# Kernel optimization log

Measured on AMD Instinct MI355X. Metric: run time of the kernel, lower is better.

## Reference

```python
import jax, jax.numpy as jnp
import numpy as np

H = 16  # n_heads from init_kwargs


def setup_inputs() -> dict:
    key = jax.random.key(0)
    ks = jax.random.split(key, 9)
    B, N, D = 4, 4096, 1024
    mk = lambda k, shape: jax.random.normal(k, shape, dtype=jnp.float32) * 0.02
    return {
        "x": jax.random.normal(ks[0], (B, N, D), dtype=jnp.float32),
        "Wq": mk(ks[1], (D, D)), "bq": mk(ks[2], (D,)),
        "Wk": mk(ks[3], (D, D)), "bk": mk(ks[4], (D,)),
        "Wv": mk(ks[5], (D, D)), "bv": mk(ks[6], (D,)),
        "Wo": mk(ks[7], (D, D)), "bo": mk(ks[8], (D,)),
    }


def _split_heads(t):
    B, N, D = t.shape
    return t.reshape(B, N, H, D // H).transpose(0, 2, 1, 3)  # b h n d


def reference(x, Wq, bq, Wk, bk, Wv, bv, Wo, bo):
    B, N, D = x.shape
    d_head = D // H
    s = (d_head ** 0.5) ** (-0.25)
    q = _split_heads(x @ Wq + bq)
    # NOTE: original computes key(x) but immediately overwrites it with
    # q.softmax(dim=-2); key projection is dead code. We replicate exactly.
    _ = x @ Wk + bk  # dead, kept for parameter-shape parity
    v = _split_heads(x @ Wv + bv)
    q = jax.nn.softmax(q, axis=-1) * s            # softmax over d_head
    k = jax.nn.softmax(q, axis=-2) * s            # softmax of q over seq dim (faithful!)
    ctx = jnp.einsum('bhnd,bhne->bhde', k, v)     # k^T @ v, [B,H,d,d]
    attn = jnp.einsum('bhnd,bhde->bhne', q, ctx)  # q @ ctx, [B,H,N,d]
    attn = attn.transpose(0, 2, 1, 3).reshape(B, N, D)
    # n_heads > 1 -> to_out linear; dropout is identity in eval mode
    return attn @ Wo + bo
```

## Files before the change

kernel.cpp:

```cpp
#include <hip/hip_runtime.h>

typedef unsigned short u16;
typedef __attribute__((ext_vector_type(8))) short short8;
typedef __attribute__((ext_vector_type(4))) float f4;
typedef __attribute__((ext_vector_type(8))) unsigned short us8;

__device__ __forceinline__ u16 f2bf(float f) {
    unsigned u = __float_as_uint(f);
    u += 0x7FFFu + ((u >> 16) & 1u);
    return (u16)(u >> 16);
}
__device__ __forceinline__ float bf2f(u16 h) {
    return __uint_as_float(((unsigned)h) << 16);
}

#define GLD16(gp, lp) __builtin_amdgcn_global_load_lds( \
    (const __attribute__((address_space(1))) void*)(gp), \
    (__attribute__((address_space(3))) void*)(lp), 16, 0, 0)

#define SCALE_S 0.594603557501360533f

__global__ __launch_bounds__(256) void convert_f32_bf16(const float* __restrict__ in,
                                                        u16* __restrict__ out) {
    const size_t i = (size_t)blockIdx.x * 256 + threadIdx.x;
    const float4* p = (const float4*)in + i * 2;
    float4 a = p[0], b = p[1];
    us8 r;
    r[0] = f2bf(a.x); r[1] = f2bf(a.y); r[2] = f2bf(a.z); r[3] = f2bf(a.w);
    r[4] = f2bf(b.x); r[5] = f2bf(b.y); r[6] = f2bf(b.z); r[7] = f2bf(b.w);
    *(us8*)(out + i * 8) = r;
}

__global__ __launch_bounds__(256) void transpose_convert3(
    const float* __restrict__ Wq, const float* __restrict__ Wv, const float* __restrict__ Wo,
    u16* __restrict__ WqvT, u16* __restrict__ WoT) {
    const float* W; u16* out;
    if (blockIdx.z == 0)      { W = Wq; out = WqvT; }
    else if (blockIdx.z == 1) { W = Wv; out = WqvT + 1024 * 1024; }
    else                      { W = Wo; out = WoT; }
    __shared__ float tile[32][33];
    const int tx = threadIdx.x, ty = threadIdx.y;
    const int x = blockIdx.x * 32 + tx;
#pragma unroll
    for (int i = 0; i < 4; ++i) {
        const int y = blockIdx.y * 32 + ty + i * 8;
        tile[ty + i * 8][tx] = W[(size_t)y * 1024 + x];
    }
    __syncthreads();
#pragma unroll
    for (int i = 0; i < 4; ++i) {
        const int yo = blockIdx.x * 32 + ty + i * 8;
        const int xo = blockIdx.y * 32 + tx;
        out[(size_t)yo * 1024 + xo] = f2bf(tile[tx][ty + i * 8]);
    }
}

__global__ void concat_bias(const float* __restrict__ bq, const float* __restrict__ bv,
                            float* __restrict__ bqv) {
    const int i = blockIdx.x * 256 + threadIdx.x;
    bqv[i] = (i < 1024) ? bq[i] : bv[i - 1024];
}

#define BAR8() do { asm volatile("" ::: "memory"); __builtin_amdgcn_s_barrier(); \
                    asm volatile("" ::: "memory"); } while (0)
#define WAITV(n) asm volatile("s_waitcnt vmcnt(" #n ")" ::: "memory")

#define STG2(arr, p, half) do { \
    const u16* s_ = (p) + (size_t)(half) * 128 * 1024; \
    u16* d_ = &arr[half][ldst]; \
    GLD16(s_, d_); \
    GLD16(s_ + (size_t)64 * 1024, d_ + 64 * 64); \
} while (0)

#define MFMA_CL(base) \
    _Pragma("unroll") for (int kk_ = 0; kk_ < 2; ++kk_) \
    _Pragma("unroll") for (int i_ = 0; i_ < 4; ++i_) \
    _Pragma("unroll") for (int j_ = 0; j_ < 4; ++j_) \
        acc[(base) + i_][j_] = __builtin_amdgcn_mfma_f32_16x16x32_bf16( \
            bf[j_][kk_], af[i_][kk_], acc[(base) + i_][j_], 0, 0, 0);

#define KTILE(AsR, BsR, AsW, BsW) do { \
    short8 bf[4][2]; \
    _Pragma("unroll") for (int j_ = 0; j_ < 4; ++j_) \
    _Pragma("unroll") for (int kk_ = 0; kk_ < 2; ++kk_) \
        bf[j_][kk_] = *(const short8*)&BsR[bhalf][(brow + j_ * 16 + lrow) * 64 + (kg0 ^ (kk_ << 5))]; \
    { \
        short8 af[4][2]; \
        _Pragma("unroll") for (int i_ = 0; i_ < 4; ++i_) \
        _Pragma("unroll") for (int kk_ = 0; kk_ < 2; ++kk_) \
            af[i_][kk_] = *(const short8*)&AsR[wrow][(i_ * 16 + lrow) * 64 + (kg0 ^ (kk_ << 5))]; \
        STG2(AsW, aP, 0); STG2(AsW, aP, 1); aP += 64; \
        __builtin_amdgcn_s_setprio(1); \
        MFMA_CL(0) \
        __builtin_amdgcn_s_setprio(0); \
    } \
    { \
        short8 af[4][2]; \
        _Pragma("unroll") for (int i_ = 0; i_ < 4; ++i_) \
        _Pragma("unroll") for (int kk_ = 0; kk_ < 2; ++kk_) \
            af[i_][kk_] = *(const short8*)&AsR[wrow][((64 + i_ * 16 + lrow)) * 64 + (kg0 ^ (kk_ << 5))]; \
        BAR8(); \
        STG2(BsW, bP, 0); STG2(BsW, bP, 1); bP += 64; \
        __builtin_amdgcn_s_setprio(1); \
        MFMA_CL(4) \
        __builtin_amdgcn_s_setprio(0); \
    } \
    WAITV(4); \
    BAR8(); \
} while (0)

#define KTILE_NOSYNC(AsR, BsR) do { \
    short8 bf[4][2]; \
    _Pragma("unroll") for (int j_ = 0; j_ < 4; ++j_) \
    _Pragma("unroll") for (int kk_ = 0; kk_ < 2; ++kk_) \
        bf[j_][kk_] = *(const short8*)&BsR[bhalf][(brow + j_ * 16 + lrow) * 64 + (kg0 ^ (kk_ << 5))]; \
    _Pragma("unroll") for (int h_ = 0; h_ < 2; ++h_) { \
        short8 af[4][2]; \
        _Pragma("unroll") for (int i_ = 0; i_ < 4; ++i_) \
        _Pragma("unroll") for (int kk_ = 0; kk_ < 2; ++kk_) \
            af[i_][kk_] = *(const short8*)&AsR[wrow][((h_ * 64 + i_ * 16 + lrow)) * 64 + (kg0 ^ (kk_ << 5))]; \
        if (h_ == 0) { MFMA_CL(0) } else { MFMA_CL(4) } \
    } \
} while (0)

__global__ __launch_bounds__(512, 2) void gemm_qv(
    const u16* __restrict__ A, const u16* __restrict__ BT,
    const float* __restrict__ bias,
    u16* __restrict__ qsOut, u16* __restrict__ vOut)
{
    __shared__ u16 As0[2][128 * 64], As1[2][128 * 64];
    __shared__ u16 Bs0[2][128 * 64], Bs1[2][128 * 64];
    const int t = threadIdx.x;
    const int l = t & 63, w = t >> 6;
    const int quad = l >> 4, lrow = l & 15;
    const int wrow = w >> 2, wcol = w & 3;
    const int bhalf = wcol >> 1, brow = (wcol & 1) * 64;

    int bx, by;
    {
        const int id = blockIdx.x + (int)gridDim.x * blockIdx.y;
        const int xcd = id & 7, j = id >> 3;
        const int xs = (int)gridDim.x >> 3;
        bx = xcd * xs + (j % xs);
        by = j / xs;
    }
    const int m0 = bx * 256, n0 = by * 256;

    const int lr0 = t >> 3;
    const int cg = ((t & 7) ^ (lr0 & 7)) * 8;
    const int ldst = lr0 * 64 + (t & 7) * 8;
    const u16* aS = A  + (size_t)(m0 + lr0) * 1024 + cg;
    const u16* bS = BT + (size_t)(n0 + lr0) * 1024 + cg;

    const int kg0 = (quad ^ (lrow & 7)) << 3;
    f4 acc[8][4] = {};

    STG2(Bs0, bS, 0); STG2(Bs0, bS, 1);
    STG2(As0, aS, 0); STG2(As0, aS, 1);
    {
        const u16* b1 = bS + 64;
        STG2(Bs1, b1, 0); STG2(Bs1, b1, 1);
    }
    WAITV(4);
    BAR8();

    const u16* aP = aS + 64;
    const u16* bP = bS + 128;

    for (int kt2 = 0; kt2 < 7; ++kt2) {
        KTILE(As0, Bs0, As1, Bs0);
        KTILE(As1, Bs1, As0, Bs1);
    }
    STG2(As1, aP, 0); STG2(As1, aP, 1);
    WAITV(0);
    BAR8();
    KTILE_NOSYNC(As0, Bs0);
    KTILE_NOSYNC(As1, Bs1);

    const int colh = n0 + wcol * 64;
    const bool isQ = n0 < 1024;
    float4 bs4[4];
#pragma unroll
    for (int j = 0; j < 4; ++j)
        bs4[j] = *(const float4*)&bias[colh + j * 16 + quad * 4];

#pragma unroll
    for (int i = 0; i < 8; ++i) {
        const int m = m0 + wrow * 128 + i * 16 + lrow;
        float v[4][4];
#pragma unroll
        for (int j = 0; j < 4; ++j) {
            v[j][0] = acc[i][j][0] + bs4[j].x;
            v[j][1] = acc[i][j][1] + bs4[j].y;
            v[j][2] = acc[i][j][2] + bs4[j].z;
            v[j][3] = acc[i][j][3] + bs4[j].w;
        }
        if (isQ) {
            float mx = v[0][0];
#pragma unroll
            for (int j = 0; j < 4; ++j)
#pragma unroll
                for (int r = 0; r < 4; ++r) mx = fmaxf(mx, v[j][r]);
            mx = fmaxf(mx, __shfl_xor(mx, 16));
            mx = fmaxf(mx, __shfl_xor(mx, 32));
            float sm = 0.f;
#pragma unroll
            for (int j = 0; j < 4; ++j)
#pragma unroll
                for (int r = 0; r < 4; ++r) { v[j][r] = __expf(v[j][r] - mx); sm += v[j][r]; }
            sm += __shfl_xor(sm, 16);
            sm += __shfl_xor(sm, 32);
            const float inv = SCALE_S / sm;
            u16* qp = qsOut + (size_t)m * 1024 + colh + quad * 4;
#pragma unroll
            for (int j = 0; j < 4; ++j) {
                uint2 pk;
                pk.x = (unsigned)f2bf(v[j][0] * inv) | ((unsigned)f2bf(v[j][1] * inv) << 16);
                pk.y = (unsigned)f2bf(v[j][2] * inv) | ((unsigned)f2bf(v[j][3] * inv) << 16);
                *(uint2*)(qp + j * 16) = pk;
            }
        } else {
            u16* vp = vOut + (size_t)m * 1024 + (colh - 1024) + quad * 4;
#pragma unroll
            for (int j = 0; j < 4; ++j) {
                uint2 pk;
                pk.x = (unsigned)f2bf(v[j][0]) | ((unsigned)f2bf(v[j][1]) << 16);
                pk.y = (unsigned)f2bf(v[j][2]) | ((unsigned)f2bf(v[j][3]) << 16);
                *(uint2*)(vp + j * 16) = pk;
            }
        }
    }
}

__global__ __launch_bounds__(512, 2) void gemm_out(
    const u16* __restrict__ A, const u16* __restrict__ BT,
    const float* __restrict__ bias, float* __restrict__ C)
{
    __shared__ u16 As0[2][128 * 64], As1[2][128 * 64];
    __shared__ u16 Bs0[2][128 * 64], Bs1[2][128 * 64];
    const int t = threadIdx.x;
    const int l = t & 63, w = t >> 6;
    const int quad = l >> 4, lrow = l & 15;
    const int wrow = w >> 2, wcol = w & 3;
    const int bhalf = wcol >> 1, brow = (wcol & 1) * 64;
    const int z = blockIdx.z;
    A  += (size_t)z * (4096 * 1024);
    BT += (size_t)z * (1024 * 1024);
    C  += (size_t)z * (4096 * 1024);

    int bx, by;
    {
        const int id = blockIdx.x + (int)gridDim.x * blockIdx.y;
        const int xcd = id & 7, j = id >> 3;
        const int xs = (int)gridDim.x >> 3;
        bx = xcd * xs + (j % xs);
        by = j / xs;
    }
    const int m0 = bx * 256, n0 = by * 256;

    const int lr0 = t >> 3;
    const int cg = ((t & 7) ^ (lr0 & 7)) * 8;
    const int ldst = lr0 * 64 + (t & 7) * 8;
    const u16* aS = A  + (size_t)(m0 + lr0) * 1024 + cg;
    const u16* bS = BT + (size_t)(n0 + lr0) * 1024 + cg;

    const int kg0 = (quad ^ (lrow & 7)) << 3;
    f4 acc[8][4] = {};

    STG2(Bs0, bS, 0); STG2(Bs0, bS, 1);
    STG2(As0, aS, 0); STG2(As0, aS, 1);
    {
        const u16* b1 = bS + 64;
        STG2(Bs1, b1, 0); STG2(Bs1, b1, 1);
    }
    WAITV(4);
    BAR8();

    const u16* aP = aS + 64;
    const u16* bP = bS + 128;

    for (int kt2 = 0; kt2 < 7; ++kt2) {
        KTILE(As0, Bs0, As1, Bs0);
        KTILE(As1, Bs1, As0, Bs1);
    }
    STG2(As1, aP, 0); STG2(As1, aP, 1);
    WAITV(0);
    BAR8();
    KTILE_NOSYNC(As0, Bs0);
    KTILE_NOSYNC(As1, Bs1);

    const int colh = n0 + wcol * 64;
    float4 bs4[4];
#pragma unroll
    for (int j = 0; j < 4; ++j)
        bs4[j] = *(const float4*)&bias[colh + j * 16 + quad * 4];
#pragma unroll
    for (int i = 0; i < 8; ++i) {
        const int m = m0 + wrow * 128 + i * 16 + lrow;
        float* cp = C + (size_t)m * 1024 + colh + quad * 4;
#pragma unroll
        for (int j = 0; j < 4; ++j) {
            float4 o;
            o.x = acc[i][j][0] + bs4[j].x;
            o.y = acc[i][j][1] + bs4[j].y;
            o.z = acc[i][j][2] + bs4[j].z;
            o.w = acc[i][j][3] + bs4[j].w;
            *(float4*)(cp + j * 16) = o;
        }
    }
}

__global__ __launch_bounds__(256) void ctx_mfma(
    const u16* __restrict__ qs, const u16* __restrict__ vb,
    float* __restrict__ Mpart, float* __restrict__ Zpart)
{
    __shared__ __align__(16) u16 Et[2][64 * 64];
    __shared__ __align__(16) u16 Vt[2][64 * 64];
    const int t = threadIdx.x;
    const int w = t >> 6, l = t & 63;
    const int quad = l >> 4, lrow = l & 15;
    const int g = blockIdx.x;
    const int split = blockIdx.y;
    const int b = g >> 4, h = g & 15;

    const int n0 = (l & 31) * 2;
    const int d0 = w * 16 + (l >> 5) * 8;
    const u16* qp = qs + ((size_t)b * 4096 + (size_t)split * 256 + n0) * 1024 + h * 64 + d0;
    const u16* vp = vb + ((size_t)b * 4096 + (size_t)split * 256 + n0) * 1024 + h * 64 + d0;

    f4 acc[4] = {};
    float zacc[8] = {};

    us8 q8a = *(const us8*)qp;
    us8 q8b = *(const us8*)(qp + 1024);
    us8 v8a = *(const us8*)vp;
    us8 v8b = *(const us8*)(vp + 1024);

    for (int slab = 0; slab < 4; ++slab) {
        unsigned epk[8], vpk[8];
#pragma unroll
        for (int j = 0; j < 8; ++j) {
            float ea = __expf(bf2f((u16)q8a[j]));
            float eb = __expf(bf2f((u16)q8b[j]));
            zacc[j] += ea + eb;
            epk[j] = (unsigned)f2bf(ea) | ((unsigned)f2bf(eb) << 16);
            vpk[j] = (unsigned)(u16)v8a[j] | ((unsigned)(u16)v8b[j] << 16);
        }
        if (slab < 3) {
            qp += 64 * 1024; vp += 64 * 1024;
            q8a = *(const us8*)qp;  q8b = *(const us8*)(qp + 1024);
            v8a = *(const us8*)vp;  v8b = *(const us8*)(vp + 1024);
        }
        u16* et = Et[slab & 1];
        u16* vt = Vt[slab & 1];
#pragma unroll
        for (int j = 0; j < 8; ++j) {
            const int d = d0 + j;
            const int off = d * 64 + (((n0 >> 3) ^ (d & 7)) << 3) + (n0 & 7);
            *(unsigned*)&et[off] = epk[j];
            *(unsigned*)&vt[off] = vpk[j];
        }
        __syncthreads();
#pragma unroll
        for (int kk = 0; kk < 2; ++kk) {
            const int blk = ((kk * 4 + quad) ^ (lrow & 7)) << 3;
            short8 a = *(const short8*)&et[(w * 16 + lrow) * 64 + blk];
#pragma unroll
            for (int j = 0; j < 4; ++j) {
                short8 bfr = *(const short8*)&vt[(j * 16 + lrow) * 64 + blk];
                acc[j] = __builtin_amdgcn_mfma_f32_16x16x32_bf16(bfr, a, acc[j], 0, 0, 0);
            }
        }
    }

#pragma unroll
    for (int j = 0; j < 8; ++j) {
        zacc[j] += __shfl_xor(zacc[j], 1);
        zacc[j] += __shfl_xor(zacc[j], 2);
        zacc[j] += __shfl_xor(zacc[j], 4);
        zacc[j] += __shfl_xor(zacc[j], 8);
        zacc[j] += __shfl_xor(zacc[j], 16);
    }
    if ((l & 31) == 0) {
        float* zp = Zpart + ((size_t)split * 64 + g) * 64 + d0;
#pragma unroll
        for (int j = 0; j < 8; ++j) zp[j] = zacc[j];
    }

    float* mp = Mpart + ((size_t)split * 64 + g) * 4096;
#pragma unroll
    for (int j = 0; j < 4; ++j) {
        float4 o;
        o.x = acc[j][0]; o.y = acc[j][1]; o.z = acc[j][2]; o.w = acc[j][3];
        *(float4*)&mp[(w * 16 + lrow) * 64 + j * 16 + quad * 4] = o;
    }
}

__global__ __launch_bounds__(256) void ctx_norm(const float* __restrict__ Mpart,
                                                const float* __restrict__ Zpart,
                                                float* __restrict__ ctx2) {
    const int g = blockIdx.x, t = threadIdx.x;
    __shared__ float rz[64];
    if (t < 64) {
        float zsum = 0.f;
#pragma unroll
        for (int s = 0; s < 16; ++s) zsum += Zpart[((size_t)s * 64 + g) * 64 + t];
        rz[t] = SCALE_S / zsum;
    }
    __syncthreads();
    for (int idx = t; idx < 4096; idx += 256) {
        float m = 0.f;
#pragma unroll
        for (int s = 0; s < 16; ++s) m += Mpart[((size_t)s * 64 + g) * 4096 + idx];
        ctx2[(size_t)g * 4096 + idx] = m * rz[idx >> 6];
    }
}

__global__ __launch_bounds__(256) void woprime(const float* __restrict__ ctx2,
                                               const u16* __restrict__ WoT,
                                               u16* __restrict__ WopT) {
    __shared__ float ctxT[64 * 65];
    __shared__ __align__(16) u16 wo[64 * 64];
    const int t = threadIdx.x;
    const int jt = blockIdx.x, h = blockIdx.y, b = blockIdx.z;
    const int g = b * 16 + h;
    for (int idx = t; idx < 4096; idx += 256) {
        const int d = idx >> 6, e = idx & 63;
        ctxT[e * 65 + d] = ctx2[(size_t)g * 4096 + idx];
    }
    const int j0 = jt * 64;
#pragma unroll
    for (int c = 0; c < 2; ++c) {
        const int ii = c * 256 + t;
        const int j = ii >> 3, c8 = ii & 7;
        *(us8*)&wo[j * 64 + c8 * 8] = *(const us8*)&WoT[(size_t)(j0 + j) * 1024 + h * 64 + c8 * 8];
    }
    __syncthreads();
    const int d = t & 63, w = t >> 6;
    float accj[16] = {};
    for (int eb = 0; eb < 8; ++eb) {
        float c8[8];
#pragma unroll
        for (int e = 0; e < 8; ++e) c8[e] = ctxT[(eb * 8 + e) * 65 + d];
#pragma unroll
        for (int jj = 0; jj < 16; ++jj) {
            us8 w8 = *(const us8*)&wo[(jj * 4 + w) * 64 + eb * 8];
#pragma unroll
            for (int e = 0; e < 8; ++e)
                accj[jj] += bf2f((u16)w8[e]) * c8[e];
        }
    }
#pragma unroll
    for (int jj = 0; jj < 16; ++jj)
        WopT[(size_t)b * 1048576 + (size_t)(j0 + jj * 4 + w) * 1024 + h * 64 + d] = f2bf(accj[jj]);
}

extern "C" void kernel_launch(void* const* d_in, const int* in_sizes, int n_in,
                              void* d_out, int out_size, void* d_ws, size_t ws_size,
                              hipStream_t stream)
{
    const float* x  = (const float*)d_in[0];
    const float* Wq = (const float*)d_in[1];
    const float* bq = (const float*)d_in[2];
    const float* Wv = (const float*)d_in[5];
    const float* bv = (const float*)d_in[6];
    const float* Wo = (const float*)d_in[7];
    const float* bo = (const float*)d_in[8];
    float* out = (float*)d_out;

    char* ws = (char*)d_ws;
    size_t o = 0;
    auto alloc = [&](size_t bytes) { char* p = ws + o; o = (o + bytes + 255) & ~(size_t)255; return p; };
    u16*   x_bf  = (u16*)  alloc(16384ull * 1024 * 2);
    u16*   WqvT  = (u16*)  alloc(2048ull * 1024 * 2);
    u16*   WoT   = (u16*)  alloc(1024ull * 1024 * 2);
    float* bqv   = (float*)alloc(2048ull * 4);
    u16*   qs    = (u16*)  alloc(16384ull * 1024 * 2);
    u16*   vbuf  = (u16*)  alloc(16384ull * 1024 * 2);
    float* Zpart = (float*)alloc(16ull * 64 * 64 * 4);
    float* ctx2  = (float*)alloc(64ull * 4096 * 4);
    u16*   WopT  = (u16*)  alloc(4ull * 1024 * 1024 * 2);
    float* Mpart = (float*)x_bf;
    (void)ws_size; (void)in_sizes; (void)n_in; (void)out_size;

    convert_f32_bf16<<<8192, 256, 0, stream>>>(x, x_bf);
    transpose_convert3<<<dim3(32, 32, 3), dim3(32, 8), 0, stream>>>(Wq, Wv, Wo, WqvT, WoT);
    concat_bias<<<8, 256, 0, stream>>>(bq, bv, bqv);

    gemm_qv<<<dim3(64, 8), 512, 0, stream>>>(x_bf, WqvT, bqv, qs, vbuf);
    ctx_mfma<<<dim3(64, 16), 256, 0, stream>>>(qs, vbuf, Mpart, Zpart);
    ctx_norm<<<64, 256, 0, stream>>>(Mpart, Zpart, ctx2);
    woprime<<<dim3(16, 16, 4), 256, 0, stream>>>(ctx2, WoT, WopT);
    gemm_out<<<dim3(16, 4, 4), 512, 0, stream>>>(qs, WopT, bo, out);
}
```

Measured before the change: 306.7 us.

## Triple-buffer A tiles in GEMM pipeline and split ctx_norm across more blocks

Both GEMM kernels now keep three LDS buffers for the A operand instead of two, so the prologue prefetches two A k-tiles and the main loop rotates through As0/As1/As2 with the wait count raised to allow more loads in flight. This aims to hide global-to-LDS latency better, at the cost of extra LDS per block (now 160 KB for two blocks per CU), which may limit occupancy. Separately, ctx_norm is launched with four times as many blocks, each handling a quarter of a head's elements, to add parallelism to a small reduction kernel.

```diff
diff --git a/kernel.cpp b/kernel.cpp
--- a/kernel.cpp
+++ b/kernel.cpp
@@ -79,7 +79,7 @@
         acc[(base) + i_][j_] = __builtin_amdgcn_mfma_f32_16x16x32_bf16( \
             bf[j_][kk_], af[i_][kk_], acc[(base) + i_][j_], 0, 0, 0);
 
-#define KTILE(AsR, BsR, AsW, BsW) do { \
+#define KTILE3(AsR, BsR, AsW, BsW) do { \
     short8 bf[4][2]; \
     _Pragma("unroll") for (int j_ = 0; j_ < 4; ++j_) \
     _Pragma("unroll") for (int kk_ = 0; kk_ < 2; ++kk_) \
@@ -105,7 +105,7 @@
         MFMA_CL(4) \
         __builtin_amdgcn_s_setprio(0); \
     } \
-    WAITV(4); \
+    WAITV(8); \
     BAR8(); \
 } while (0)
 
@@ -123,12 +123,36 @@
     } \
 } while (0)
 
+#define GEMM_PRO_AND_LOOP() \
+    STG2(Bs0, bS, 0); STG2(Bs0, bS, 1); \
+    STG2(As0, aS, 0); STG2(As0, aS, 1); \
+    { const u16* b1 = bS + 64; STG2(Bs1, b1, 0); STG2(Bs1, b1, 1); } \
+    { const u16* a1 = aS + 64; STG2(As1, a1, 0); STG2(As1, a1, 1); } \
+    WAITV(8); \
+    BAR8(); \
+    const u16* aP = aS + 128; \
+    const u16* bP = bS + 128; \
+    for (int it6 = 0; it6 < 2; ++it6) { \
+        KTILE3(As0, Bs0, As2, Bs0); \
+        KTILE3(As1, Bs1, As0, Bs1); \
+        KTILE3(As2, Bs0, As1, Bs0); \
+        KTILE3(As0, Bs1, As2, Bs1); \
+        KTILE3(As1, Bs0, As0, Bs0); \
+        KTILE3(As2, Bs1, As1, Bs1); \
+    } \
+    KTILE3(As0, Bs0, As2, Bs0);   \
+    KTILE3(As1, Bs1, As0, Bs1);   \
+    WAITV(0); \
+    BAR8(); \
+    KTILE_NOSYNC(As2, Bs0);       \
+    KTILE_NOSYNC(As0, Bs1);
+
 __global__ __launch_bounds__(512, 2) void gemm_qv(
     const u16* __restrict__ A, const u16* __restrict__ BT,
     const float* __restrict__ bias,
     u16* __restrict__ qsOut, u16* __restrict__ vOut)
 {
-    __shared__ u16 As0[2][128 * 64], As1[2][128 * 64];
+    __shared__ u16 As0[2][128 * 64], As1[2][128 * 64], As2[2][128 * 64];
     __shared__ u16 Bs0[2][128 * 64], Bs1[2][128 * 64];
     const int t = threadIdx.x;
     const int l = t & 63, w = t >> 6;
@@ -155,27 +179,7 @@
     const int kg0 = (quad ^ (lrow & 7)) << 3;
     f4 acc[8][4] = {};
 
-    STG2(Bs0, bS, 0); STG2(Bs0, bS, 1);
-    STG2(As0, aS, 0); STG2(As0, aS, 1);
-    {
-        const u16* b1 = bS + 64;
-        STG2(Bs1, b1, 0); STG2(Bs1, b1, 1);
-    }
-    WAITV(4);
-    BAR8();
-
-    const u16* aP = aS + 64;
-    const u16* bP = bS + 128;
-
-    for (int kt2 = 0; kt2 < 7; ++kt2) {
-        KTILE(As0, Bs0, As1, Bs0);
-        KTILE(As1, Bs1, As0, Bs1);
-    }
-    STG2(As1, aP, 0); STG2(As1, aP, 1);
-    WAITV(0);
-    BAR8();
-    KTILE_NOSYNC(As0, Bs0);
-    KTILE_NOSYNC(As1, Bs1);
+    GEMM_PRO_AND_LOOP()
 
     const int colh = n0 + wcol * 64;
     const bool isQ = n0 < 1024;
@@ -236,7 +240,7 @@
     const u16* __restrict__ A, const u16* __restrict__ BT,
     const float* __restrict__ bias, float* __restrict__ C)
 {
-    __shared__ u16 As0[2][128 * 64], As1[2][128 * 64];
+    __shared__ u16 As0[2][128 * 64], As1[2][128 * 64], As2[2][128 * 64];
     __shared__ u16 Bs0[2][128 * 64], Bs1[2][128 * 64];
     const int t = threadIdx.x;
     const int l = t & 63, w = t >> 6;
@@ -267,27 +271,7 @@
     const int kg0 = (quad ^ (lrow & 7)) << 3;
     f4 acc[8][4] = {};
 
-    STG2(Bs0, bS, 0); STG2(Bs0, bS, 1);
-    STG2(As0, aS, 0); STG2(As0, aS, 1);
-    {
-        const u16* b1 = bS + 64;
-        STG2(Bs1, b1, 0); STG2(Bs1, b1, 1);
-    }
-    WAITV(4);
-    BAR8();
-
-    const u16* aP = aS + 64;
-    const u16* bP = bS + 128;
-
-    for (int kt2 = 0; kt2 < 7; ++kt2) {
-        KTILE(As0, Bs0, As1, Bs0);
-        KTILE(As1, Bs1, As0, Bs1);
-    }
-    STG2(As1, aP, 0); STG2(As1, aP, 1);
-    WAITV(0);
-    BAR8();
-    KTILE_NOSYNC(As0, Bs0);
-    KTILE_NOSYNC(As1, Bs1);
+    GEMM_PRO_AND_LOOP()
 
     const int colh = n0 + wcol * 64;
     float4 bs4[4];
@@ -399,7 +383,7 @@
 __global__ __launch_bounds__(256) void ctx_norm(const float* __restrict__ Mpart,
                                                 const float* __restrict__ Zpart,
                                                 float* __restrict__ ctx2) {
-    const int g = blockIdx.x, t = threadIdx.x;
+    const int g = blockIdx.x >> 2, q = blockIdx.x & 3, t = threadIdx.x;
     __shared__ float rz[64];
     if (t < 64) {
         float zsum = 0.f;
@@ -408,7 +392,9 @@
         rz[t] = SCALE_S / zsum;
     }
     __syncthreads();
-    for (int idx = t; idx < 4096; idx += 256) {
+    const int base = q * 1024;
+    for (int ii = t; ii < 1024; ii += 256) {
+        const int idx = base + ii;
         float m = 0.f;
 #pragma unroll
         for (int s = 0; s < 16; ++s) m += Mpart[((size_t)s * 64 + g) * 4096 + idx];
@@ -489,7 +475,7 @@
 
     gemm_qv<<<dim3(64, 8), 512, 0, stream>>>(x_bf, WqvT, bqv, qs, vbuf);
     ctx_mfma<<<dim3(64, 16), 256, 0, stream>>>(qs, vbuf, Mpart, Zpart);
-    ctx_norm<<<64, 256, 0, stream>>>(Mpart, Zpart, ctx2);
+    ctx_norm<<<256, 256, 0, stream>>>(Mpart, Zpart, ctx2);
     woprime<<<dim3(16, 16, 4), 256, 0, stream>>>(ctx2, WoT, WopT);
     gemm_out<<<dim3(16, 4, 4), 512, 0, stream>>>(qs, WopT, bo, out);
 }
```

After: 300.2 us. 1.02x faster.
